# Kernel optimization log

Hardware: AMD Instinct MI355X
Metric: run time of the kernel (lower is better)

The kernel has to match this reference:

```python
import jax, jax.numpy as jnp
import numpy as np
from jax.scipy.linalg import solve_triangular

N, K, D = 131072, 8, 32  # samples, clusters, dims


def setup_inputs() -> dict:
    key = jax.random.key(0)
    k1, k2, k3, k4 = jax.random.split(key, 4)
    return {
        "X": jax.random.normal(k1, (N, D), dtype=jnp.float32),
        "mu": jax.random.normal(k2, (K, D), dtype=jnp.float32),
        "L": jax.random.normal(k3, (K, D, D), dtype=jnp.float32),
        "weights": jax.random.normal(k4, (K,), dtype=jnp.float32),
        "it": 0,
    }


def _mixture_log_likelihoods(X, mu, L, weights):
    K_, D_ = mu.shape
    LOG2PI = float(np.log(2.0 * np.pi))
    # update_covariances: A_k = L_k L_k^T + I  (always SPD -> cholesky succeeds)
    A = jnp.einsum('kab,kcb->kac', L, L) + jnp.eye(D_, dtype=L.dtype)
    Lc = jnp.linalg.cholesky(A)            # [K,D,D] lower Cholesky factors
    invLc = jnp.linalg.inv(Lc)             # [K,D,D]
    # all cluster pairs (cartesian_prod order: i outer, j inner)
    ii, jj = [g.reshape(-1) for g in jnp.meshgrid(jnp.arange(K_), jnp.arange(K_), indexing='ij')]
    Si, Sj = Lc[ii], Lc[jj]                # NOTE: original uses the CHOLESKY FACTORS here
    invSi, invSj = invLc[ii], invLc[jj]
    mui, muj = mu[ii], mu[jj]
    # _gaussian_product: sigma = inv(inv(Si)+inv(Sj)); mu = sigma @ (inv(Si) mu_i + inv(Sj) mu_j)
    sigma = jnp.linalg.inv(invSi + invSj)                      # [P,D,D]
    rhs = jnp.einsum('pab,pb->pa', invSi, mui) + jnp.einsum('pab,pb->pa', invSj, muj)
    mu_p = jnp.einsum('pab,pb->pa', sigma, rhs)                # [P,D]
    # _product_z: log(1/sqrt(det(2*pi*(Si+Sj))) * exp(-0.5 dmu^T inv(Si+Sj) dmu))
    S = Si + Sj
    dmu = mui - muj
    quad = -0.5 * jnp.einsum('pa,pab,pb->p', dmu, jnp.linalg.inv(S), dmu)
    z = -0.5 * jnp.log(jnp.linalg.det(2.0 * np.pi * S)) + quad  # [P]
    # _unormalised_pdf: lower-triangular solve against sigma (only lower triangle used)
    diff = X[None, :, :] - mu_p[:, None, :]                    # [P,N,D]
    m = solve_triangular(sigma, jnp.swapaxes(diff, 1, 2), lower=True)  # [P,D,N]
    ll = -0.5 * (jnp.sum(m * m, axis=1) + D_ * LOG2PI
                 + jnp.log(jnp.linalg.det(sigma))[:, None])    # [P,N]
    logw = jax.nn.log_softmax(weights)                         # softmax weights, then log
    logprob = z[:, None] + ll + logw[ii][:, None] + logw[jj][:, None]  # [P,N]
    return jnp.log(jnp.sum(jnp.exp(logprob), axis=0))          # [N]


def reference(X, mu, L, weights, it):
    ll = _mixture_log_likelihoods(X, mu, L, weights)
    return jax.scipy.special.logsumexp(ll, axis=0)  # scalar
```

## Files before the change

kernel.cpp:

```cpp
#include <hip/hip_runtime.h>

#define D 32
#define K 8
#define NPAIR 36

#define AFROFF 0
#define WFROFF 8192
#define C2OFF 8448
#define CMAXOFF 8484
#define TICKOFF 8488
#define LCOFF 8512
#define PARTOFF 16704

typedef short s16x8 __attribute__((ext_vector_type(8)));
typedef float f32x16 __attribute__((ext_vector_type(16)));

union FragU { uint4 u4; s16x8 s8; };

__host__ __device__ constexpr int gidx(int i, int j) {
    return i * 8 + j - i * (i + 1) / 2;
}

static __device__ inline unsigned short f2bf(float v) {
    union { float f; unsigned u; } c; c.f = v;
    unsigned r = (c.u + 0x7FFFu + ((c.u >> 16) & 1u)) >> 16;
    return (unsigned short)r;
}
static __device__ inline float bf2f(unsigned short h) {
    union { unsigned u; float f; } c; c.u = ((unsigned)h) << 16;
    return c.f;
}

static __device__ inline void pack8(const float* v, uint4& hi, uint4& lo) {
    unsigned hw[4], lw[4];
    #pragma unroll
    for (int p = 0; p < 4; ++p) {
        const unsigned short h0 = f2bf(v[2 * p]);
        const unsigned short h1 = f2bf(v[2 * p + 1]);
        hw[p] = (unsigned)h0 | ((unsigned)h1 << 16);
        lw[p] = (unsigned)f2bf(v[2 * p] - bf2f(h0))
              | ((unsigned)f2bf(v[2 * p + 1] - bf2f(h1)) << 16);
    }
    hi = make_uint4(hw[0], hw[1], hw[2], hw[3]);
    lo = make_uint4(lw[0], lw[1], lw[2], lw[3]);
}

__global__ __launch_bounds__(64) void setup1_kernel(
    const float* __restrict__ mu, const float* __restrict__ L,
    float* __restrict__ ws)
{
    __shared__ float sA[D][D + 1];
    __shared__ float sLc[D][D + 1];
    __shared__ float sI[D][D + 1];
    __shared__ float sWv[D];
    const int k = blockIdx.x;
    const int tid = threadIdx.x;
    const int i = tid & 31;
    const int row = tid & 31;
    const int hg = tid >> 5;

    for (int e = tid; e < D * D; e += 64) sI[e >> 5][e & 31] = L[k * D * D + e];
    __syncthreads();

    for (int e = tid; e < D * D; e += 64) {
        const int a = e >> 5, c = e & 31;
        float s = (a == c) ? 1.0f : 0.0f;
        #pragma unroll
        for (int b = 0; b < D; ++b) s = fmaf(sI[a][b], sI[c][b], s);
        sA[a][c] = s;
    }
    __syncthreads();

    float lrow[D];
    #pragma unroll
    for (int j = 0; j < D; ++j) {
        if (i == j) {
            float s = sA[j][j];
            #pragma unroll
            for (int b = 0; b < j; ++b) s = fmaf(-lrow[b], lrow[b], s);
            const float d = sqrtf(s);
            lrow[j] = d;
            #pragma unroll
            for (int b = 0; b < j; ++b) sLc[j][b] = lrow[b];
            sLc[j][j] = d;
        }
        __syncthreads();
        if (i > j) {
            float s = sA[i][j];
            #pragma unroll
            for (int b = 0; b < j; ++b) s = fmaf(-lrow[b], sLc[j][b], s);
            lrow[j] = s / sLc[j][j];
        }
    }
    __syncthreads();

    for (int e = tid; e < D * D; e += 64) {
        const int r = e >> 5, c = e & 31;
        ws[LCOFF + k * D * D + e] = (c <= r) ? sLc[r][c] : 0.0f;
    }

    {
        const int j = i;
        #pragma unroll
        for (int ii = 0; ii < D; ++ii) {
            float s = (ii == j) ? 1.0f : 0.0f;
            #pragma unroll
            for (int b = 0; b < ii; ++b) s = fmaf(-sLc[ii][b], sI[b][j], s);
            sI[ii][j] = s / sLc[ii][ii];
        }
    }
    __syncthreads();

    {
        float s = 0.0f;
        #pragma unroll
        for (int b = 0; b < D; ++b) s = fmaf(sI[i][b], mu[k * D + b], s);
        if (tid < 32) sWv[i] = s;
    }

    #pragma unroll
    for (int s = 0; s < 2; ++s) {
        float v[8];
        #pragma unroll
        for (int e = 0; e < 8; ++e) v[e] = sI[row][16 * s + 8 * hg + e];
        uint4 hi, lo;
        pack8(v, hi, lo);
        *(uint4*)((char*)ws + AFROFF * 4 + k * 4096 + ((s * 2 + 0) * 64 + tid) * 16) = hi;
        *(uint4*)((char*)ws + AFROFF * 4 + k * 4096 + ((s * 2 + 1) * 64 + tid) * 16) = lo;
    }
    __syncthreads();

    if (tid < 32) {
        const int h = tid >> 4, r = tid & 15;
        ws[WFROFF + k * 32 + h * 16 + r] = -sWv[(r & 3) + 8 * (r >> 2) + 4 * h];
    }
}

#define SLC(kk, r, c) sLc2[(kk) * 1024 + (r) * 32 + (c)]

__global__ __launch_bounds__(256) void setup2_kernel(
    const float* __restrict__ mu, const float* __restrict__ weights,
    float* __restrict__ ws)
{
    __shared__ float sLc2[K * D * D];
    __shared__ float sMu[K * D];
    __shared__ float sWt[K];
    __shared__ float sLogw[K];
    __shared__ float sCp[NPAIR];
    __shared__ float sCmax;
    const int tid = threadIdx.x;

    {
        const float4* src = (const float4*)(ws + LCOFF);
        float4* dst = (float4*)sLc2;
        #pragma unroll
        for (int e = 0; e < 8; ++e) dst[tid + 256 * e] = src[tid + 256 * e];
        sMu[tid] = mu[tid];
        if (tid < K) sWt[tid] = weights[tid];
    }
    __syncthreads();

    if (tid == 0) {
        float m = -INFINITY;
        for (int t = 0; t < K; ++t) m = fmaxf(m, sWt[t]);
        float s = 0.0f;
        for (int t = 0; t < K; ++t) s += expf(sWt[t] - m);
        const float lse = m + logf(s);
        for (int t = 0; t < K; ++t) sLogw[t] = sWt[t] - lse;
        *(unsigned int*)(ws + TICKOFF) = 0u;
    }
    __syncthreads();

    if (tid < NPAIR) {
        int tt = tid, pi = 0;
        while (tt >= (K - pi)) { tt -= (K - pi); ++pi; }
        const int pj = pi + tt;
        const float LOG2PI = 1.8378770664093453f;
        float sumlogS = 0.0f, logdetsig = 0.0f;
        #pragma unroll
        for (int r = 0; r < D; ++r) {
            const float di = SLC(pi, r, r), dj = SLC(pj, r, r);
            sumlogS += logf(di + dj);
            logdetsig -= logf(1.0f / di + 1.0f / dj);
        }
        float v[D];
        float quad_acc = 0.0f;
        #pragma unroll
        for (int r = 0; r < D; ++r) {
            const float d0 = sMu[pi * D + r] - sMu[pj * D + r];
            float s = d0;
            #pragma unroll
            for (int b = 0; b < r; ++b)
                s = fmaf(-(SLC(pi, r, b) + SLC(pj, r, b)), v[b], s);
            v[r] = s / (SLC(pi, r, r) + SLC(pj, r, r));
            quad_acc = fmaf(d0, v[r], quad_acc);
        }
        const float quad = -0.5f * quad_acc;
        float c = quad - 0.5f * sumlogS - (float)D * LOG2PI - 0.5f * logdetsig
                  + sLogw[pi] + sLogw[pj];
        if (pi < pj) c += 0.6931471805599453f;
        sCp[tid] = c;
    }
    __syncthreads();
    if (tid == 0) {
        float m = -INFINITY;
        for (int t = 0; t < NPAIR; ++t) m = fmaxf(m, sCp[t]);
        sCmax = m;
        ws[CMAXOFF] = m;
    }
    __syncthreads();
    if (tid < NPAIR)
        ws[C2OFF + tid] = (sCp[tid] - sCmax) * 1.4426950408889634f;
}

__global__ __launch_bounds__(256) void main_kernel(
    const float* __restrict__ X, const float* __restrict__ cst,
    float* __restrict__ partials, float* __restrict__ out,
    unsigned int* __restrict__ ticket, int nsamp, int nblk)
{
    __shared__ float sRed[4];
    __shared__ int sIsLast;
    const int tid = threadIdx.x;
    const int wv = tid >> 6;
    const int lane = tid & 63;
    const int col = lane & 31;
    const int hg = lane >> 5;

    const int n = blockIdx.x * 128 + wv * 32 + col;
    const int m = (n < nsamp) ? n : 0;

    FragU bh0, bl0, bh1, bl1;
    {
        const float4 a0 = *(const float4*)(X + m * D + 8 * hg);
        const float4 a1 = *(const float4*)(X + m * D + 8 * hg + 4);
        const float4 a2 = *(const float4*)(X + m * D + 16 + 8 * hg);
        const float4 a3 = *(const float4*)(X + m * D + 16 + 8 * hg + 4);
        float v0[8] = {a0.x, a0.y, a0.z, a0.w, a1.x, a1.y, a1.z, a1.w};
        float v1[8] = {a2.x, a2.y, a2.z, a2.w, a3.x, a3.y, a3.z, a3.w};
        pack8(v0, bh0.u4, bl0.u4);
        pack8(v1, bh1.u4, bl1.u4);
    }

    const char* afr = (const char*)cst;
    const float* wfr = cst + WFROFF;

    f32x16 yk[K];
    #pragma unroll
    for (int k = 0; k < K; ++k) {
        FragU ah0, al0, ah1, al1;
        ah0.u4 = *(const uint4*)(afr + k * 4096 + (0 * 64 + lane) * 16);
        al0.u4 = *(const uint4*)(afr + k * 4096 + (1 * 64 + lane) * 16);
        ah1.u4 = *(const uint4*)(afr + k * 4096 + (2 * 64 + lane) * 16);
        al1.u4 = *(const uint4*)(afr + k * 4096 + (3 * 64 + lane) * 16);

        f32x16 acc1;
        {
            const float4* wp = (const float4*)(wfr + k * 32 + hg * 16);
            const float4 w0 = wp[0], w1 = wp[1], w2 = wp[2], w3 = wp[3];
            acc1[0] = w0.x;  acc1[1] = w0.y;  acc1[2] = w0.z;  acc1[3] = w0.w;
            acc1[4] = w1.x;  acc1[5] = w1.y;  acc1[6] = w1.z;  acc1[7] = w1.w;
            acc1[8] = w2.x;  acc1[9] = w2.y;  acc1[10] = w2.z; acc1[11] = w2.w;
            acc1[12] = w3.x; acc1[13] = w3.y; acc1[14] = w3.z; acc1[15] = w3.w;
        }
        f32x16 acc2 = (f32x16)(0.0f);

        acc1 = __builtin_amdgcn_mfma_f32_32x32x16_bf16(ah0.s8, bh0.s8, acc1, 0, 0, 0);
        acc2 = __builtin_amdgcn_mfma_f32_32x32x16_bf16(al1.s8, bh1.s8, acc2, 0, 0, 0);
        acc1 = __builtin_amdgcn_mfma_f32_32x32x16_bf16(ah1.s8, bh1.s8, acc1, 0, 0, 0);
        acc2 = __builtin_amdgcn_mfma_f32_32x32x16_bf16(ah0.s8, bl0.s8, acc2, 0, 0, 0);
        acc1 = __builtin_amdgcn_mfma_f32_32x32x16_bf16(al0.s8, bh0.s8, acc1, 0, 0, 0);
        acc2 = __builtin_amdgcn_mfma_f32_32x32x16_bf16(ah1.s8, bl1.s8, acc2, 0, 0, 0);

        yk[k] = acc1 + acc2;
    }

    float G[NPAIR];
    #pragma unroll
    for (int pi = 0; pi < K; ++pi)
        #pragma unroll
        for (int pj = pi; pj < K; ++pj) {
            float g = 0.0f;
            #pragma unroll
            for (int r = 0; r < 16; ++r)
                g = fmaf(yk[pi][r], yk[pj][r], g);
            G[gidx(pi, pj)] = g;
        }

    float accs = 0.0f;
    const float NH = -0.72134752044448170f;
    #pragma unroll
    for (int pi = 0; pi < K; ++pi)
        #pragma unroll
        for (int pj = pi; pj < K; ++pj) {
            const float q = 2.0f * G[gidx(pi, pj)]
                          + G[gidx(pi, pi)] + G[gidx(pj, pj)];
            const float qf = q + __shfl_xor(q, 32, 64);
            accs += exp2f(fmaf(NH, qf, cst[C2OFF + gidx(pi, pj)]));
        }
    accs = (n < nsamp) ? accs : 0.0f;

    #pragma unroll
    for (int s = 1; s < 64; s <<= 1) accs += __shfl_xor(accs, s, 64);
    if (lane == 0) sRed[wv] = 0.5f * accs;
    __syncthreads();

    if (tid == 0) {
        const float blocksum = sRed[0] + sRed[1] + sRed[2] + sRed[3];
        partials[blockIdx.x] = blocksum;
        __threadfence();
        const unsigned prev = atomicAdd(ticket, 1u);
        sIsLast = (prev == (unsigned)(nblk - 1)) ? 1 : 0;
    }
    __syncthreads();

    if (sIsLast) {
        __threadfence();
        float a2 = 0.0f;
        for (int e = tid; e < nblk; e += 256) a2 += partials[e];
        #pragma unroll
        for (int s = 1; s < 64; s <<= 1) a2 += __shfl_xor(a2, s, 64);
        if ((tid & 63) == 0) sRed[tid >> 6] = a2;
        __syncthreads();
        if (tid == 0)
            out[0] = cst[CMAXOFF]
                   + logf(sRed[0] + sRed[1] + sRed[2] + sRed[3]);
    }
}

extern "C" void kernel_launch(void* const* d_in, const int* in_sizes, int n_in,
                              void* d_out, int out_size, void* d_ws, size_t ws_size,
                              hipStream_t stream) {
    const float* X = (const float*)d_in[0];
    const float* mu = (const float*)d_in[1];
    const float* L = (const float*)d_in[2];
    const float* w = (const float*)d_in[3];
    float* wsf = (float*)d_ws;
    float* out = (float*)d_out;

    const int nsamp = in_sizes[0] / D;
    const int nblk = (nsamp + 127) / 128;

    setup1_kernel<<<K, 64, 0, stream>>>(mu, L, wsf);
    setup2_kernel<<<1, 256, 0, stream>>>(mu, w, wsf);
    main_kernel<<<nblk, 256, 0, stream>>>(X, wsf, wsf + PARTOFF, out,
                                          (unsigned int*)(wsf + TICKOFF),
                                          nsamp, nblk);
}
```

Measured before the change: 151.1 us.

## Switch main kernel to 16x16x32 MFMA with per-cluster centered inputs

The main kernel now uses 16x16x32 bf16 MFMAs on 16 samples per wave instead of 32x32x16 on 32 samples. It subtracts each cluster mean from X before the split-bf16 pack, where before the bias was folded into the accumulator init. The per-k Gram is computed inline with diagonal terms precomputed, so the large 36-entry G array goes away. The change aims to cut register pressure and raise occupancy, but it adds an extra cross-lane shuffle per pair, repeats the bf16 pack per cluster, and doubles the grid size.

Measured after the change: 239.7 us. +58.6%, slower.

```diff
diff --git a/kernel.cpp b/kernel.cpp
--- a/kernel.cpp
+++ b/kernel.cpp
@@ -5,15 +5,14 @@
 #define NPAIR 36
 
 #define AFROFF 0
-#define WFROFF 8192
-#define C2OFF 8448
-#define CMAXOFF 8484
-#define TICKOFF 8488
-#define LCOFF 8512
-#define PARTOFF 16704
+#define C2OFF 8192
+#define CMAXOFF 8228
+#define TICKOFF 8232
+#define LCOFF 8240
+#define PARTOFF 16448
 
 typedef short s16x8 __attribute__((ext_vector_type(8)));
-typedef float f32x16 __attribute__((ext_vector_type(16)));
+typedef float f32x4 __attribute__((ext_vector_type(4)));
 
 union FragU { uint4 u4; s16x8 s8; };
 
@@ -52,12 +51,9 @@
     __shared__ float sA[D][D + 1];
     __shared__ float sLc[D][D + 1];
     __shared__ float sI[D][D + 1];
-    __shared__ float sWv[D];
     const int k = blockIdx.x;
     const int tid = threadIdx.x;
     const int i = tid & 31;
-    const int row = tid & 31;
-    const int hg = tid >> 5;
 
     for (int e = tid; e < D * D; e += 64) sI[e >> 5][e & 31] = L[k * D * D + e];
     __syncthreads();
@@ -111,28 +107,17 @@
     }
     __syncthreads();
 
-    {
-        float s = 0.0f;
-        #pragma unroll
-        for (int b = 0; b < D; ++b) s = fmaf(sI[i][b], mu[k * D + b], s);
-        if (tid < 32) sWv[i] = s;
-    }
-
-    #pragma unroll
-    for (int s = 0; s < 2; ++s) {
+    #pragma unroll
+    for (int rb = 0; rb < 2; ++rb) {
         float v[8];
         #pragma unroll
-        for (int e = 0; e < 8; ++e) v[e] = sI[row][16 * s + 8 * hg + e];
+        for (int e = 0; e < 8; ++e)
+            v[e] = sI[rb * 16 + (tid & 15)][(tid >> 4) * 8 + e];
         uint4 hi, lo;
         pack8(v, hi, lo);
-        *(uint4*)((char*)ws + AFROFF * 4 + k * 4096 + ((s * 2 + 0) * 64 + tid) * 16) = hi;
-        *(uint4*)((char*)ws + AFROFF * 4 + k * 4096 + ((s * 2 + 1) * 64 + tid) * 16) = lo;
-    }
-    __syncthreads();
-
-    if (tid < 32) {
-        const int h = tid >> 4, r = tid & 15;
-        ws[WFROFF + k * 32 + h * 16 + r] = -sWv[(r & 3) + 8 * (r >> 2) + 4 * h];
+        char* base = (char*)ws + k * 4096;
+        *(uint4*)(base + (rb * 2 + 0) * 1024 + tid * 16) = hi;
+        *(uint4*)(base + (rb * 2 + 1) * 1024 + tid * 16) = lo;
     }
 }
 
@@ -214,7 +199,8 @@
 }
 
 __global__ __launch_bounds__(256) void main_kernel(
-    const float* __restrict__ X, const float* __restrict__ cst,
+    const float* __restrict__ X, const float* __restrict__ mu,
+    const float* __restrict__ cst,
     float* __restrict__ partials, float* __restrict__ out,
     unsigned int* __restrict__ ticket, int nsamp, int nblk)
 {
@@ -223,68 +209,67 @@
     const int tid = threadIdx.x;
     const int wv = tid >> 6;
     const int lane = tid & 63;
-    const int col = lane & 31;
-    const int hg = lane >> 5;
-
-    const int n = blockIdx.x * 128 + wv * 32 + col;
+    const int col = lane & 15;
+    const int g = lane >> 4;
+
+    const int n = blockIdx.x * 64 + wv * 16 + col;
     const int m = (n < nsamp) ? n : 0;
 
-    FragU bh0, bl0, bh1, bl1;
+    float xr[8];
     {
-        const float4 a0 = *(const float4*)(X + m * D + 8 * hg);
-        const float4 a1 = *(const float4*)(X + m * D + 8 * hg + 4);
-        const float4 a2 = *(const float4*)(X + m * D + 16 + 8 * hg);
-        const float4 a3 = *(const float4*)(X + m * D + 16 + 8 * hg + 4);
-        float v0[8] = {a0.x, a0.y, a0.z, a0.w, a1.x, a1.y, a1.z, a1.w};
-        float v1[8] = {a2.x, a2.y, a2.z, a2.w, a3.x, a3.y, a3.z, a3.w};
-        pack8(v0, bh0.u4, bl0.u4);
-        pack8(v1, bh1.u4, bl1.u4);
+        const float4 a0 = *(const float4*)(X + m * D + g * 8);
+        const float4 a1 = *(const float4*)(X + m * D + g * 8 + 4);
+        xr[0] = a0.x; xr[1] = a0.y; xr[2] = a0.z; xr[3] = a0.w;
+        xr[4] = a1.x; xr[5] = a1.y; xr[6] = a1.z; xr[7] = a1.w;
     }
 
     const char* afr = (const char*)cst;
-    const float* wfr = cst + WFROFF;
-
-    f32x16 yk[K];
+
+    f32x4 yk0[K], yk1[K];
     #pragma unroll
     for (int k = 0; k < K; ++k) {
+        float b[8];
+        {
+            const float4 m40 = *(const float4*)(mu + k * D + g * 8);
+            const float4 m41 = *(const float4*)(mu + k * D + g * 8 + 4);
+            b[0] = xr[0] - m40.x; b[1] = xr[1] - m40.y;
+            b[2] = xr[2] - m40.z; b[3] = xr[3] - m40.w;
+            b[4] = xr[4] - m41.x; b[5] = xr[5] - m41.y;
+            b[6] = xr[6] - m41.z; b[7] = xr[7] - m41.w;
+        }
+        FragU bh, bl;
+        pack8(b, bh.u4, bl.u4);
+
         FragU ah0, al0, ah1, al1;
-        ah0.u4 = *(const uint4*)(afr + k * 4096 + (0 * 64 + lane) * 16);
-        al0.u4 = *(const uint4*)(afr + k * 4096 + (1 * 64 + lane) * 16);
-        ah1.u4 = *(const uint4*)(afr + k * 4096 + (2 * 64 + lane) * 16);
-        al1.u4 = *(const uint4*)(afr + k * 4096 + (3 * 64 + lane) * 16);
-
-        f32x16 acc1;
-        {
-            const float4* wp = (const float4*)(wfr + k * 32 + hg * 16);
-            const float4 w0 = wp[0], w1 = wp[1], w2 = wp[2], w3 = wp[3];
-            acc1[0] = w0.x;  acc1[1] = w0.y;  acc1[2] = w0.z;  acc1[3] = w0.w;
-            acc1[4] = w1.x;  acc1[5] = w1.y;  acc1[6] = w1.z;  acc1[7] = w1.w;
-            acc1[8] = w2.x;  acc1[9] = w2.y;  acc1[10] = w2.z; acc1[11] = w2.w;
-            acc1[12] = w3.x; acc1[13] = w3.y; acc1[14] = w3.z; acc1[15] = w3.w;
-        }
-        f32x16 acc2 = (f32x16)(0.0f);
-
-        acc1 = __builtin_amdgcn_mfma_f32_32x32x16_bf16(ah0.s8, bh0.s8, acc1, 0, 0, 0);
-        acc2 = __builtin_amdgcn_mfma_f32_32x32x16_bf16(al1.s8, bh1.s8, acc2, 0, 0, 0);
-        acc1 = __builtin_amdgcn_mfma_f32_32x32x16_bf16(ah1.s8, bh1.s8, acc1, 0, 0, 0);
-        acc2 = __builtin_amdgcn_mfma_f32_32x32x16_bf16(ah0.s8, bl0.s8, acc2, 0, 0, 0);
-        acc1 = __builtin_amdgcn_mfma_f32_32x32x16_bf16(al0.s8, bh0.s8, acc1, 0, 0, 0);
-        acc2 = __builtin_amdgcn_mfma_f32_32x32x16_bf16(ah1.s8, bl1.s8, acc2, 0, 0, 0);
-
-        yk[k] = acc1 + acc2;
-    }
-
-    float G[NPAIR];
-    #pragma unroll
-    for (int pi = 0; pi < K; ++pi)
-        #pragma unroll
-        for (int pj = pi; pj < K; ++pj) {
-            float g = 0.0f;
-            #pragma unroll
-            for (int r = 0; r < 16; ++r)
-                g = fmaf(yk[pi][r], yk[pj][r], g);
-            G[gidx(pi, pj)] = g;
-        }
+        const char* base = afr + k * 4096 + lane * 16;
+        ah0.u4 = *(const uint4*)(base);
+        al0.u4 = *(const uint4*)(base + 1024);
+        ah1.u4 = *(const uint4*)(base + 2048);
+        al1.u4 = *(const uint4*)(base + 3072);
+
+        f32x4 p0 = (f32x4)(0.0f), q0 = (f32x4)(0.0f);
+        f32x4 p1 = (f32x4)(0.0f), q1 = (f32x4)(0.0f);
+        p0 = __builtin_amdgcn_mfma_f32_16x16x32_bf16(ah0.s8, bh.s8, p0, 0, 0, 0);
+        q0 = __builtin_amdgcn_mfma_f32_16x16x32_bf16(al0.s8, bh.s8, q0, 0, 0, 0);
+        p1 = __builtin_amdgcn_mfma_f32_16x16x32_bf16(ah1.s8, bh.s8, p1, 0, 0, 0);
+        q1 = __builtin_amdgcn_mfma_f32_16x16x32_bf16(al1.s8, bh.s8, q1, 0, 0, 0);
+        q0 = __builtin_amdgcn_mfma_f32_16x16x32_bf16(ah0.s8, bl.s8, q0, 0, 0, 0);
+        q1 = __builtin_amdgcn_mfma_f32_16x16x32_bf16(ah1.s8, bl.s8, q1, 0, 0, 0);
+        yk0[k] = p0 + q0;
+        yk1[k] = p1 + q1;
+    }
+
+    float dg[K];
+    #pragma unroll
+    for (int k = 0; k < K; ++k) {
+        float s = 0.0f;
+        #pragma unroll
+        for (int r = 0; r < 4; ++r) {
+            s = fmaf(yk0[k][r], yk0[k][r], s);
+            s = fmaf(yk1[k][r], yk1[k][r], s);
+        }
+        dg[k] = s;
+    }
 
     float accs = 0.0f;
     const float NH = -0.72134752044448170f;
@@ -292,16 +277,22 @@
     for (int pi = 0; pi < K; ++pi)
         #pragma unroll
         for (int pj = pi; pj < K; ++pj) {
-            const float q = 2.0f * G[gidx(pi, pj)]
-                          + G[gidx(pi, pi)] + G[gidx(pj, pj)];
-            const float qf = q + __shfl_xor(q, 32, 64);
+            float p = 0.0f;
+            #pragma unroll
+            for (int r = 0; r < 4; ++r) {
+                p = fmaf(yk0[pi][r], yk0[pj][r], p);
+                p = fmaf(yk1[pi][r], yk1[pj][r], p);
+            }
+            const float q = 2.0f * p + dg[pi] + dg[pj];
+            const float t = q + __shfl_xor(q, 16, 64);
+            const float qf = t + __shfl_xor(t, 32, 64);
             accs += exp2f(fmaf(NH, qf, cst[C2OFF + gidx(pi, pj)]));
         }
     accs = (n < nsamp) ? accs : 0.0f;
 
     #pragma unroll
     for (int s = 1; s < 64; s <<= 1) accs += __shfl_xor(accs, s, 64);
-    if (lane == 0) sRed[wv] = 0.5f * accs;
+    if (lane == 0) sRed[wv] = 0.25f * accs;
     __syncthreads();
 
     if (tid == 0) {
@@ -338,11 +329,11 @@
     float* out = (float*)d_out;
 
     const int nsamp = in_sizes[0] / D;
-    const int nblk = (nsamp + 127) / 128;
+    const int nblk = (nsamp + 63) / 64;
 
     setup1_kernel<<<K, 64, 0, stream>>>(mu, L, wsf);
     setup2_kernel<<<1, 256, 0, stream>>>(mu, w, wsf);
-    main_kernel<<<nblk, 256, 0, stream>>>(X, wsf, wsf + PARTOFF, out,
+    main_kernel<<<nblk, 256, 0, stream>>>(X, mu, wsf, wsf + PARTOFF, out,
                                           (unsigned int*)(wsf + TICKOFF),
                                           nsamp, nblk);
 }
```
